# Optimization experiments

Measured on AMD Instinct MI355X. Metric: run time of the kernel, lower is better.

The kernel has to match this reference:

```python
import jax, jax.numpy as jnp
import numpy as np

B, T, C = 32, 128, 64
E, H = 8, 4            # feat_dim, num_heads
D = E // H             # head_dim = 2
HID = 32               # hidden_dim


def setup_inputs() -> dict:
    key = jax.random.key(0)
    ks = jax.random.split(key, 20)
    s = 0.1
    return {
        "x": jax.random.normal(ks[0], (B, T, C), jnp.float32),
        # input_proj: Linear(C, C)
        "W_in": jax.random.normal(ks[1], (C, C), jnp.float32) * s,
        "b_in": jax.random.normal(ks[2], (C,), jnp.float32) * s,
        # time_step_score: Linear(C, C//4) -> GELU -> Linear(C//4, 1) -> Sigmoid
        "W_ts1": jax.random.normal(ks[3], (C // 4, C), jnp.float32) * s,
        "b_ts1": jax.random.normal(ks[4], (C // 4,), jnp.float32) * s,
        "W_ts2": jax.random.normal(ks[5], (1, C // 4), jnp.float32) * s,
        "b_ts2": jax.random.normal(ks[6], (1,), jnp.float32) * s,
        # per-channel GRU(1 -> E): torch gate order (r, z, n)
        "W_ih": jax.random.normal(ks[7], (C, 3 * E), jnp.float32) * s,      # input size 1
        "W_hh": jax.random.normal(ks[8], (C, 3 * E, E), jnp.float32) * s,
        "b_ih": jax.random.normal(ks[9], (C, 3 * E), jnp.float32) * s,
        "b_hh": jax.random.normal(ks[10], (C, 3 * E), jnp.float32) * s,
        # shared MultiheadAttention(E, 4): packed in_proj + out_proj
        "W_qkv": jax.random.normal(ks[11], (3 * E, E), jnp.float32) * s,
        "b_qkv": jax.random.normal(ks[12], (3 * E,), jnp.float32) * s,
        "W_o": jax.random.normal(ks[13], (E, E), jnp.float32) * s,
        "b_o": jax.random.normal(ks[14], (E,), jnp.float32) * s,
        # out_proj: Linear(C*E, HID)
        "W_out": jax.random.normal(ks[15], (HID, C * E), jnp.float32) * s,
        "b_out": jax.random.normal(ks[16], (HID,), jnp.float32) * s,
    }


def _forward(x, W_in, b_in, W_ts1, b_ts1, W_ts2, b_ts2,
             W_ih, W_hh, b_ih, b_hh, W_qkv, b_qkv, W_o, b_o, W_out, b_out):
    bs, ts, c = x.shape
    # time step importance: per-timestep MLP over the raw features
    h1 = jax.nn.gelu(jnp.einsum('btc,fc->btf', x, W_ts1) + b_ts1, approximate=False)
    ts_imp = jax.nn.sigmoid(jnp.einsum('btf,of->bto', h1, W_ts2) + b_ts2)[..., 0]  # [B,T]

    xp = jnp.einsum('btc,dc->btd', x, W_in) + b_in  # [B,T,C]

    # Batched per-channel GRU scan over time. state h: [B,C,E]
    def step(h, x_t):
        gi = x_t[:, :, None] * W_ih[None] + b_ih          # [B,C,3E]
        gh = jnp.einsum('bce,cge->bcg', h, W_hh) + b_hh   # [B,C,3E]
        ir, iz, inn = gi[..., :E], gi[..., E:2 * E], gi[..., 2 * E:]
        hr, hz, hn = gh[..., :E], gh[..., E:2 * E], gh[..., 2 * E:]
        r = jax.nn.sigmoid(ir + hr)
        z = jax.nn.sigmoid(iz + hz)
        n = jnp.tanh(inn + r * hn)
        h_new = (1.0 - z) * n + z * h
        return h_new, h_new

    h0 = jnp.zeros((bs, c, E), xp.dtype)
    _, hs = jax.lax.scan(step, h0, jnp.transpose(xp, (1, 0, 2)))  # [T,B,C,E]
    hs_bcte = jnp.transpose(hs, (1, 2, 0, 3))                     # [B,C,T,E]

    # Shared MHA applied independently per channel (batched over B*C)
    qkv = jnp.einsum('bcte,fe->bctf', hs_bcte, W_qkv) + b_qkv     # [B,C,T,3E]
    q, k, v = qkv[..., :E], qkv[..., E:2 * E], qkv[..., 2 * E:]
    def heads(t):
        return t.reshape(bs, c, ts, H, D)
    q, k, v = heads(q), heads(k), heads(v)
    scores = jnp.einsum('bcthd,bcshd->bchts', q, k) / np.sqrt(D)
    attn = jax.nn.softmax(scores, axis=-1)
    o = jnp.einsum('bchts,bcshd->bcthd', attn, v).reshape(bs, c, ts, E)
    attn_out = jnp.einsum('bcte,fe->bctf', o, W_o) + b_o          # [B,C,T,E]
    attention = jnp.transpose(attn_out, (0, 2, 1, 3))             # [B,T,C,E]

    out_flat = jnp.transpose(hs, (1, 0, 2, 3)).reshape(bs, ts, c * E)  # [B,T,C*E]
    out = jnp.einsum('btf,hf->bth', out_flat, W_out) + b_out           # [B,T,HID]

    feat_imp = jax.nn.sigmoid(attention.sum(axis=(1, 3)))   # [B,C]
    tsf_imp = jax.nn.sigmoid(attention.sum(axis=-1))        # [B,T,C]
    return out[:, -1, :], feat_imp, ts_imp, tsf_imp


def reference(x, W_in, b_in, W_ts1, b_ts1, W_ts2, b_ts2,
              W_ih, W_hh, b_ih, b_hh, W_qkv, b_qkv, W_o, b_o, W_out, b_out):
    return _forward(x, W_in, b_in, W_ts1, b_ts1, W_ts2, b_ts2,
                    W_ih, W_hh, b_ih, b_hh, W_qkv, b_qkv, W_o, b_o, W_out, b_out)
```

## Files before the change

### kernel.cpp

```cpp
#include <hip/hip_runtime.h>
#include <hip/hip_bf16.h>
#include <math.h>

#define B_ 32
#define T_ 128
#define C_ 64
#define E_ 8
#define HID_ 32

__device__ __forceinline__ float sigmoidf_(float x) { return 1.0f / (1.0f + __expf(-x)); }
__device__ __forceinline__ float tanhf_(float x) {
    float xc = fminf(fmaxf(x, -15.0f), 15.0f);
    float e = __expf(2.0f * xc);
    return (e - 1.0f) / (e + 1.0f);
}

__global__ __launch_bounds__(64) void k_gru(
    const float* __restrict__ x, const float* __restrict__ W_in, const float* __restrict__ b_in,
    const float* __restrict__ W_ih, const float* __restrict__ W_hh,
    const float* __restrict__ b_ih, const float* __restrict__ b_hh,
    float* __restrict__ hs, float* __restrict__ fh)
{
    const int tid = threadIdx.x;
    const int ci = tid >> 3;
    const int e = tid & 7;
    const int chain = blockIdx.x * 8 + ci;
    const int b = chain >> 6;
    const int c = chain & 63;

    __shared__ float wsh[8][C_];
    __shared__ float xc[8][T_ + 1];

#pragma unroll
    for (int i = 0; i < 8; ++i) {
        int idx = tid * 8 + i;
        int ci2 = idx >> 6;
        int cc = (blockIdx.x * 8 + ci2) & 63;
        wsh[ci2][idx & 63] = W_in[cc * C_ + (idx & 63)];
    }
    __syncthreads();

    const float bi = b_in[c];
    for (int tt = 0; tt < 16; ++tt) {
        const int t = e * 16 + tt;
        const float4* xr = (const float4*)(x + (b * T_ + t) * C_);
        float a = bi;
#pragma unroll
        for (int k4 = 0; k4 < 16; ++k4) {
            float4 xv = xr[k4];
            a = fmaf(xv.x, wsh[ci][k4 * 4 + 0], a);
            a = fmaf(xv.y, wsh[ci][k4 * 4 + 1], a);
            a = fmaf(xv.z, wsh[ci][k4 * 4 + 2], a);
            a = fmaf(xv.w, wsh[ci][k4 * 4 + 3], a);
        }
        xc[ci][t] = a;
    }
    __syncthreads();

    float wr[E_], wz[E_], wn[E_];
#pragma unroll
    for (int j = 0; j < E_; ++j) {
        wr[j] = W_hh[(c * 24 + 0 * E_ + e) * E_ + j];
        wz[j] = W_hh[(c * 24 + 1 * E_ + e) * E_ + j];
        wn[j] = W_hh[(c * 24 + 2 * E_ + e) * E_ + j];
    }
    const float wir = W_ih[c * 24 + e], wiz = W_ih[c * 24 + E_ + e], win = W_ih[c * 24 + 2 * E_ + e];
    const float bir = b_ih[c * 24 + e], biz = b_ih[c * 24 + E_ + e], bin_ = b_ih[c * 24 + 2 * E_ + e];
    const float bhr = b_hh[c * 24 + e], bhz = b_hh[c * 24 + E_ + e], bhn = b_hh[c * 24 + 2 * E_ + e];

    float h = 0.0f;
    float* ho = hs + (size_t)chain * T_ * E_ + e;
    for (int t = 0; t < T_; ++t) {
        float xv = xc[ci][t];
        float gr = fmaf(xv, wir, bir) + bhr;
        float gz = fmaf(xv, wiz, biz) + bhz;
        float gn = fmaf(xv, win, bin_);
        float hn = bhn;
#pragma unroll
        for (int j = 0; j < E_; ++j) {
            float hj = __shfl(h, j, E_);
            gr = fmaf(hj, wr[j], gr);
            gz = fmaf(hj, wz[j], gz);
            hn = fmaf(hj, wn[j], hn);
        }
        float r = sigmoidf_(gr);
        float z = sigmoidf_(gz);
        float nn = tanhf_(fmaf(r, hn, gn));
        h = (1.0f - z) * nn + z * h;
        ho[t * E_] = h;
    }
    fh[chain * E_ + e] = h;
}

__global__ __launch_bounds__(256) void k_attn(
    const float* __restrict__ hs, const float* __restrict__ W_qkv, const float* __restrict__ b_qkv,
    const float* __restrict__ W_o, const float* __restrict__ b_o,
    float* __restrict__ feat_imp, float* __restrict__ tsf_imp)
{
    const int bc = blockIdx.x;
    const int b = bc >> 6, c = bc & 63;
    const int tid = threadIdx.x;
    const int t = tid & 127;
    const int p = tid >> 7;

    __shared__ __align__(16) float ks[T_][E_];
    __shared__ __align__(16) float vs[T_][E_];
    __shared__ __align__(16) float pacc[T_][12];
    __shared__ float wssum[E_];
    __shared__ float bsum_s;
    __shared__ float red[T_];

    float hrow[E_];
    {
        const float4* hp = (const float4*)(hs + (size_t)bc * T_ * E_ + t * E_);
        float4 h0 = hp[0], h1 = hp[1];
        hrow[0] = h0.x; hrow[1] = h0.y; hrow[2] = h0.z; hrow[3] = h0.w;
        hrow[4] = h1.x; hrow[5] = h1.y; hrow[6] = h1.z; hrow[7] = h1.w;
    }

    const float qscale = 0.70710678118654752f * 1.44269504088896341f;
    float q[E_];
#pragma unroll
    for (int f = 0; f < E_; ++f) {
        float a = b_qkv[f];
#pragma unroll
        for (int j = 0; j < E_; ++j) a = fmaf(hrow[j], W_qkv[f * E_ + j], a);
        q[f] = a * qscale;
    }
    if (p == 0) {
#pragma unroll
        for (int f = 0; f < E_; ++f) {
            float a = b_qkv[E_ + f];
#pragma unroll
            for (int j = 0; j < E_; ++j) a = fmaf(hrow[j], W_qkv[(E_ + f) * E_ + j], a);
            ks[t][f] = a;
        }
    } else {
#pragma unroll
        for (int f = 0; f < E_; ++f) {
            float a = b_qkv[2 * E_ + f];
#pragma unroll
            for (int j = 0; j < E_; ++j) a = fmaf(hrow[j], W_qkv[(2 * E_ + f) * E_ + j], a);
            vs[t][f] = a;
        }
    }
    if (tid < E_) {
        float ws = 0.0f;
#pragma unroll
        for (int fp = 0; fp < E_; ++fp) ws += W_o[fp * E_ + tid];
        wssum[tid] = ws;
    }
    if (tid == E_) {
        float bs = 0.0f;
#pragma unroll
        for (int fp = 0; fp < E_; ++fp) bs += b_o[fp];
        bsum_s = bs;
    }
    __syncthreads();

    float l[4] = {0.f, 0.f, 0.f, 0.f};
    float acc[E_] = {0.f, 0.f, 0.f, 0.f, 0.f, 0.f, 0.f, 0.f};
    const int s0 = p * 64;
    for (int s = s0; s < s0 + 64; ++s) {
        float4 k0 = *(const float4*)&ks[s][0];
        float4 k1 = *(const float4*)&ks[s][4];
        float4 v0 = *(const float4*)&vs[s][0];
        float4 v1 = *(const float4*)&vs[s][4];
        float p0 = exp2f(fmaf(q[1], k0.y, q[0] * k0.x));
        float p1 = exp2f(fmaf(q[3], k0.w, q[2] * k0.z));
        float p2 = exp2f(fmaf(q[5], k1.y, q[4] * k1.x));
        float p3 = exp2f(fmaf(q[7], k1.w, q[6] * k1.z));
        l[0] += p0; l[1] += p1; l[2] += p2; l[3] += p3;
        acc[0] = fmaf(p0, v0.x, acc[0]); acc[1] = fmaf(p0, v0.y, acc[1]);
        acc[2] = fmaf(p1, v0.z, acc[2]); acc[3] = fmaf(p1, v0.w, acc[3]);
        acc[4] = fmaf(p2, v1.x, acc[4]); acc[5] = fmaf(p2, v1.y, acc[5]);
        acc[6] = fmaf(p3, v1.z, acc[6]); acc[7] = fmaf(p3, v1.w, acc[7]);
    }

    if (p == 1) {
#pragma unroll
        for (int i = 0; i < 4; ++i) pacc[t][i] = l[i];
#pragma unroll
        for (int j = 0; j < 8; ++j) pacc[t][4 + j] = acc[j];
    }
    __syncthreads();

    if (p == 0) {
#pragma unroll
        for (int i = 0; i < 4; ++i) l[i] += pacc[t][i];
#pragma unroll
        for (int j = 0; j < 8; ++j) acc[j] += pacc[t][4 + j];
        float S = bsum_s;
#pragma unroll
        for (int f = 0; f < E_; ++f) S = fmaf(acc[f] / l[f >> 1], wssum[f], S);
        tsf_imp[(size_t)b * T_ * C_ + (size_t)t * C_ + c] = sigmoidf_(S);
        red[t] = S;
    }
    __syncthreads();
    for (int off = 64; off > 0; off >>= 1) {
        if (p == 0 && t < off) red[t] += red[t + off];
        __syncthreads();
    }
    if (tid == 0) feat_imp[bc] = sigmoidf_(red[0]);
}

__global__ __launch_bounds__(64) void k_ts(
    const float* __restrict__ x,
    const float* __restrict__ W_ts1, const float* __restrict__ b_ts1,
    const float* __restrict__ W_ts2, const float* __restrict__ b_ts2,
    float* __restrict__ ts_imp)
{
    const int bt = blockIdx.x;
    const int tid = threadIdx.x;
    __shared__ float xs[C_];
    __shared__ float h1[16];
    xs[tid] = x[bt * C_ + tid];
    __syncthreads();
    if (tid < 16) {
        float a = b_ts1[tid];
#pragma unroll
        for (int k = 0; k < C_; ++k) a = fmaf(xs[k], W_ts1[tid * C_ + k], a);
        h1[tid] = 0.5f * a * (1.0f + erff(a * 0.70710678118654752f));
    }
    __syncthreads();
    if (tid == 0) {
        float s = b_ts2[0];
#pragma unroll
        for (int k = 0; k < 16; ++k) s = fmaf(h1[k], W_ts2[k], s);
        ts_imp[bt] = sigmoidf_(s);
    }
}

__global__ __launch_bounds__(64) void k_out(
    const float* __restrict__ fh, const float* __restrict__ W_out, const float* __restrict__ b_out,
    float* __restrict__ out0)
{
    const int b = blockIdx.x;
    const int tid = threadIdx.x;
    __shared__ float hf[C_ * E_];
    const float4* src = (const float4*)(fh + (b * C_ + tid) * E_);
    float4* dst = (float4*)(hf + tid * E_);
    dst[0] = src[0];
    dst[1] = src[1];
    __syncthreads();
    if (tid < HID_) {
        float a = b_out[tid];
        const float* wo = W_out + tid * (C_ * E_);
        for (int k = 0; k < C_ * E_; ++k) a = fmaf(hf[k], wo[k], a);
        out0[b * HID_ + tid] = a;
    }
}

extern "C" void kernel_launch(void* const* d_in, const int* in_sizes, int n_in,
                              void* d_out, int out_size, void* d_ws, size_t ws_size,
                              hipStream_t stream) {
    (void)in_sizes; (void)n_in; (void)out_size; (void)ws_size;

    float* out0 = (float*)d_out;
    float* feat = out0 + B_ * HID_;
    float* tsim = feat + B_ * C_;
    float* tsf  = tsim + B_ * T_;

    const float* x     = (const float*)d_in[0];
    const float* W_in  = (const float*)d_in[1];
    const float* b_in  = (const float*)d_in[2];
    const float* W_ts1 = (const float*)d_in[3];
    const float* b_ts1 = (const float*)d_in[4];
    const float* W_ts2 = (const float*)d_in[5];
    const float* b_ts2 = (const float*)d_in[6];
    const float* W_ih  = (const float*)d_in[7];
    const float* W_hh  = (const float*)d_in[8];
    const float* b_ih  = (const float*)d_in[9];
    const float* b_hh  = (const float*)d_in[10];
    const float* W_qkv = (const float*)d_in[11];
    const float* b_qkv = (const float*)d_in[12];
    const float* W_o   = (const float*)d_in[13];
    const float* b_o   = (const float*)d_in[14];
    const float* W_out = (const float*)d_in[15];
    const float* b_out = (const float*)d_in[16];

    float* fhb = (float*)d_ws;
    float* hsb = fhb + B_ * C_ * E_;

    hipLaunchKernelGGL(k_gru, dim3(B_ * C_ / 8), dim3(64), 0, stream,
                       x, W_in, b_in, W_ih, W_hh, b_ih, b_hh, hsb, fhb);
    hipLaunchKernelGGL(k_attn, dim3(B_ * C_), dim3(256), 0, stream,
                       hsb, W_qkv, b_qkv, W_o, b_o, feat, tsf);
    hipLaunchKernelGGL(k_ts, dim3(B_ * T_), dim3(64), 0, stream,
                       x, W_ts1, b_ts1, W_ts2, b_ts2, tsim);
    hipLaunchKernelGGL(k_out, dim3(B_), dim3(64), 0, stream,
                       fhb, W_out, b_out, out0);
}
```

Measured before the change: 101.8 us.

## Halve attention block threads with two queries per thread and fast math intrinsics

The attention kernel now runs 128 threads per (b,c) instead of 256. Each thread computes K/V for one row, then handles two query rows over half the key range. The two halves are combined with xor shuffles instead of a shared-memory partial buffer and an extra barrier, so each K/V shared load is reused across two queries. Sigmoid and tanh in the GRU and elsewhere now use exp2 plus a hardware reciprocal, and the GRU update is folded into one fma; this trims the serial recurrence latency but slightly reduces numerical accuracy.

```diff
diff --git a/kernel.cpp b/kernel.cpp
--- a/kernel.cpp
+++ b/kernel.cpp
@@ -8,11 +8,16 @@
 #define E_ 8
 #define HID_ 32
 
-__device__ __forceinline__ float sigmoidf_(float x) { return 1.0f / (1.0f + __expf(-x)); }
-__device__ __forceinline__ float tanhf_(float x) {
+#define LOG2E 1.44269504088896341f
+
+__device__ __forceinline__ float fast_rcp(float x) { return __builtin_amdgcn_rcpf(x); }
+__device__ __forceinline__ float fast_sigmoid(float x) {
+    return fast_rcp(1.0f + exp2f(-LOG2E * x));
+}
+__device__ __forceinline__ float fast_tanh(float x) {
     float xc = fminf(fmaxf(x, -15.0f), 15.0f);
-    float e = __expf(2.0f * xc);
-    return (e - 1.0f) / (e + 1.0f);
+    float t = exp2f(2.0f * LOG2E * xc);
+    return (t - 1.0f) * fast_rcp(t + 1.0f);
 }
 
 __global__ __launch_bounds__(64) void k_gru(
@@ -83,16 +88,16 @@
             gz = fmaf(hj, wz[j], gz);
             hn = fmaf(hj, wn[j], hn);
         }
-        float r = sigmoidf_(gr);
-        float z = sigmoidf_(gz);
-        float nn = tanhf_(fmaf(r, hn, gn));
-        h = (1.0f - z) * nn + z * h;
+        float r = fast_sigmoid(gr);
+        float z = fast_sigmoid(gz);
+        float nn = fast_tanh(fmaf(r, hn, gn));
+        h = fmaf(z, h - nn, nn);
         ho[t * E_] = h;
     }
     fh[chain * E_ + e] = h;
 }
 
-__global__ __launch_bounds__(256) void k_attn(
+__global__ __launch_bounds__(128) void k_attn(
     const float* __restrict__ hs, const float* __restrict__ W_qkv, const float* __restrict__ b_qkv,
     const float* __restrict__ W_o, const float* __restrict__ b_o,
     float* __restrict__ feat_imp, float* __restrict__ tsf_imp)
@@ -100,108 +105,128 @@
     const int bc = blockIdx.x;
     const int b = bc >> 6, c = bc & 63;
     const int tid = threadIdx.x;
-    const int t = tid & 127;
-    const int p = tid >> 7;
-
+    const int r = tid >> 1;
+    const int p = tid & 1;
+
+    __shared__ __align__(16) float hsl[T_][E_];
     __shared__ __align__(16) float ks[T_][E_];
     __shared__ __align__(16) float vs[T_][E_];
-    __shared__ __align__(16) float pacc[T_][12];
     __shared__ float wssum[E_];
     __shared__ float bsum_s;
     __shared__ float red[T_];
 
-    float hrow[E_];
     {
-        const float4* hp = (const float4*)(hs + (size_t)bc * T_ * E_ + t * E_);
-        float4 h0 = hp[0], h1 = hp[1];
-        hrow[0] = h0.x; hrow[1] = h0.y; hrow[2] = h0.z; hrow[3] = h0.w;
-        hrow[4] = h1.x; hrow[5] = h1.y; hrow[6] = h1.z; hrow[7] = h1.w;
-    }
-
-    const float qscale = 0.70710678118654752f * 1.44269504088896341f;
-    float q[E_];
-#pragma unroll
-    for (int f = 0; f < E_; ++f) {
-        float a = b_qkv[f];
-#pragma unroll
-        for (int j = 0; j < E_; ++j) a = fmaf(hrow[j], W_qkv[f * E_ + j], a);
-        q[f] = a * qscale;
-    }
-    if (p == 0) {
+        const float4* hp = (const float4*)(hs + (size_t)bc * T_ * E_ + tid * E_);
+        ((float4*)&hsl[tid][0])[0] = hp[0];
+        ((float4*)&hsl[tid][0])[1] = hp[1];
+    }
+    if (tid < E_) {
+        float ws = 0.0f;
+#pragma unroll
+        for (int fp = 0; fp < E_; ++fp) ws += W_o[fp * E_ + tid];
+        wssum[tid] = ws;
+    }
+    if (tid == E_) {
+        float bs = 0.0f;
+#pragma unroll
+        for (int fp = 0; fp < E_; ++fp) bs += b_o[fp];
+        bsum_s = bs;
+    }
+    __syncthreads();
+
+    const float qscale = 0.70710678118654752f * LOG2E;
+    {
+        float hr[E_];
+#pragma unroll
+        for (int j = 0; j < E_; ++j) hr[j] = hsl[tid][j];
 #pragma unroll
         for (int f = 0; f < E_; ++f) {
             float a = b_qkv[E_ + f];
 #pragma unroll
-            for (int j = 0; j < E_; ++j) a = fmaf(hrow[j], W_qkv[(E_ + f) * E_ + j], a);
-            ks[t][f] = a;
-        }
-    } else {
+            for (int j = 0; j < E_; ++j) a = fmaf(hr[j], W_qkv[(E_ + f) * E_ + j], a);
+            ks[tid][f] = a;
+        }
 #pragma unroll
         for (int f = 0; f < E_; ++f) {
             float a = b_qkv[2 * E_ + f];
 #pragma unroll
-            for (int j = 0; j < E_; ++j) a = fmaf(hrow[j], W_qkv[(2 * E_ + f) * E_ + j], a);
-            vs[t][f] = a;
-        }
-    }
-    if (tid < E_) {
-        float ws = 0.0f;
-#pragma unroll
-        for (int fp = 0; fp < E_; ++fp) ws += W_o[fp * E_ + tid];
-        wssum[tid] = ws;
-    }
-    if (tid == E_) {
-        float bs = 0.0f;
-#pragma unroll
-        for (int fp = 0; fp < E_; ++fp) bs += b_o[fp];
-        bsum_s = bs;
-    }
-    __syncthreads();
-
-    float l[4] = {0.f, 0.f, 0.f, 0.f};
-    float acc[E_] = {0.f, 0.f, 0.f, 0.f, 0.f, 0.f, 0.f, 0.f};
-    const int s0 = p * 64;
-    for (int s = s0; s < s0 + 64; ++s) {
-        float4 k0 = *(const float4*)&ks[s][0];
-        float4 k1 = *(const float4*)&ks[s][4];
-        float4 v0 = *(const float4*)&vs[s][0];
-        float4 v1 = *(const float4*)&vs[s][4];
-        float p0 = exp2f(fmaf(q[1], k0.y, q[0] * k0.x));
-        float p1 = exp2f(fmaf(q[3], k0.w, q[2] * k0.z));
-        float p2 = exp2f(fmaf(q[5], k1.y, q[4] * k1.x));
-        float p3 = exp2f(fmaf(q[7], k1.w, q[6] * k1.z));
-        l[0] += p0; l[1] += p1; l[2] += p2; l[3] += p3;
-        acc[0] = fmaf(p0, v0.x, acc[0]); acc[1] = fmaf(p0, v0.y, acc[1]);
-        acc[2] = fmaf(p1, v0.z, acc[2]); acc[3] = fmaf(p1, v0.w, acc[3]);
-        acc[4] = fmaf(p2, v1.x, acc[4]); acc[5] = fmaf(p2, v1.y, acc[5]);
-        acc[6] = fmaf(p3, v1.z, acc[6]); acc[7] = fmaf(p3, v1.w, acc[7]);
-    }
-
-    if (p == 1) {
-#pragma unroll
-        for (int i = 0; i < 4; ++i) pacc[t][i] = l[i];
-#pragma unroll
-        for (int j = 0; j < 8; ++j) pacc[t][4 + j] = acc[j];
-    }
-    __syncthreads();
-
-    if (p == 0) {
-#pragma unroll
-        for (int i = 0; i < 4; ++i) l[i] += pacc[t][i];
-#pragma unroll
-        for (int j = 0; j < 8; ++j) acc[j] += pacc[t][4 + j];
-        float S = bsum_s;
-#pragma unroll
-        for (int f = 0; f < E_; ++f) S = fmaf(acc[f] / l[f >> 1], wssum[f], S);
-        tsf_imp[(size_t)b * T_ * C_ + (size_t)t * C_ + c] = sigmoidf_(S);
-        red[t] = S;
-    }
+            for (int j = 0; j < E_; ++j) a = fmaf(hr[j], W_qkv[(2 * E_ + f) * E_ + j], a);
+            vs[tid][f] = a;
+        }
+    }
+    float q0[E_], q1[E_];
+#pragma unroll
+    for (int f = 0; f < E_; ++f) {
+        float a0 = b_qkv[f], a1 = b_qkv[f];
+#pragma unroll
+        for (int j = 0; j < E_; ++j) {
+            float w = W_qkv[f * E_ + j];
+            a0 = fmaf(hsl[r][j], w, a0);
+            a1 = fmaf(hsl[r + 64][j], w, a1);
+        }
+        q0[f] = a0 * qscale;
+        q1[f] = a1 * qscale;
+    }
+    __syncthreads();
+
+    float l0[4] = {0.f,0.f,0.f,0.f}, l1[4] = {0.f,0.f,0.f,0.f};
+    float a0[E_] = {0.f,0.f,0.f,0.f,0.f,0.f,0.f,0.f};
+    float a1[E_] = {0.f,0.f,0.f,0.f,0.f,0.f,0.f,0.f};
+    const float* kb = &ks[p * 64][0];
+    const float* vb = &vs[p * 64][0];
+#pragma unroll 8
+    for (int i = 0; i < 64; ++i) {
+        float4 k0 = *(const float4*)(kb + i * 8);
+        float4 k1 = *(const float4*)(kb + i * 8 + 4);
+        float4 v0 = *(const float4*)(vb + i * 8);
+        float4 v1 = *(const float4*)(vb + i * 8 + 4);
+        float p00 = exp2f(fmaf(q0[1], k0.y, q0[0] * k0.x));
+        float p01 = exp2f(fmaf(q0[3], k0.w, q0[2] * k0.z));
+        float p02 = exp2f(fmaf(q0[5], k1.y, q0[4] * k1.x));
+        float p03 = exp2f(fmaf(q0[7], k1.w, q0[6] * k1.z));
+        float p10 = exp2f(fmaf(q1[1], k0.y, q1[0] * k0.x));
+        float p11 = exp2f(fmaf(q1[3], k0.w, q1[2] * k0.z));
+        float p12 = exp2f(fmaf(q1[5], k1.y, q1[4] * k1.x));
+        float p13 = exp2f(fmaf(q1[7], k1.w, q1[6] * k1.z));
+        l0[0] += p00; l0[1] += p01; l0[2] += p02; l0[3] += p03;
+        l1[0] += p10; l1[1] += p11; l1[2] += p12; l1[3] += p13;
+        a0[0] = fmaf(p00, v0.x, a0[0]); a0[1] = fmaf(p00, v0.y, a0[1]);
+        a0[2] = fmaf(p01, v0.z, a0[2]); a0[3] = fmaf(p01, v0.w, a0[3]);
+        a0[4] = fmaf(p02, v1.x, a0[4]); a0[5] = fmaf(p02, v1.y, a0[5]);
+        a0[6] = fmaf(p03, v1.z, a0[6]); a0[7] = fmaf(p03, v1.w, a0[7]);
+        a1[0] = fmaf(p10, v0.x, a1[0]); a1[1] = fmaf(p10, v0.y, a1[1]);
+        a1[2] = fmaf(p11, v0.z, a1[2]); a1[3] = fmaf(p11, v0.w, a1[3]);
+        a1[4] = fmaf(p12, v1.x, a1[4]); a1[5] = fmaf(p12, v1.y, a1[5]);
+        a1[6] = fmaf(p13, v1.z, a1[6]); a1[7] = fmaf(p13, v1.w, a1[7]);
+    }
+
+#pragma unroll
+    for (int i = 0; i < 4; ++i) {
+        l0[i] += __shfl_xor(l0[i], 1);
+        l1[i] += __shfl_xor(l1[i], 1);
+    }
+#pragma unroll
+    for (int j = 0; j < E_; ++j) {
+        a0[j] += __shfl_xor(a0[j], 1);
+        a1[j] += __shfl_xor(a1[j], 1);
+    }
+
+    const float* lm = p ? l1 : l0;
+    const float* am = p ? a1 : a0;
+    const int row = p ? (r + 64) : r;
+    float S = bsum_s;
+#pragma unroll
+    for (int f = 0; f < E_; ++f)
+        S = fmaf(am[f] * fast_rcp(lm[f >> 1]), wssum[f], S);
+
+    tsf_imp[(size_t)b * T_ * C_ + (size_t)row * C_ + c] = fast_sigmoid(S);
+    red[row] = S;
     __syncthreads();
     for (int off = 64; off > 0; off >>= 1) {
-        if (p == 0 && t < off) red[t] += red[t + off];
+        if (tid < off) red[tid] += red[tid + off];
         __syncthreads();
     }
-    if (tid == 0) feat_imp[bc] = sigmoidf_(red[0]);
+    if (tid == 0) feat_imp[bc] = fast_sigmoid(red[0]);
 }
 
 __global__ __launch_bounds__(64) void k_ts(
@@ -227,7 +252,7 @@
         float s = b_ts2[0];
 #pragma unroll
         for (int k = 0; k < 16; ++k) s = fmaf(h1[k], W_ts2[k], s);
-        ts_imp[bt] = sigmoidf_(s);
+        ts_imp[bt] = fast_sigmoid(s);
     }
 }
 
@@ -284,7 +309,7 @@
 
     hipLaunchKernelGGL(k_gru, dim3(B_ * C_ / 8), dim3(64), 0, stream,
                        x, W_in, b_in, W_ih, W_hh, b_ih, b_hh, hsb, fhb);
-    hipLaunchKernelGGL(k_attn, dim3(B_ * C_), dim3(256), 0, stream,
+    hipLaunchKernelGGL(k_attn, dim3(B_ * C_), dim3(128), 0, stream,
                        hsb, W_qkv, b_qkv, W_o, b_o, feat, tsf);
     hipLaunchKernelGGL(k_ts, dim3(B_ * T_), dim3(64), 0, stream,
                        x, W_ts1, b_ts1, W_ts2, b_ts2, tsim);
```

After: 110.6 us. +8.7%, slower.

## Fold W_o column sums into V and use fast reciprocal sigmoid/tanh

Applied to the files above, without the earlier changes.

In the attention kernel, each head's V pair is pre-combined with the summed W_o columns into one scalar per head. The softmax-weighted accumulation then needs 4 accumulators instead of 8, V shared memory shrinks, and the partial-sum exchange is smaller. The W_o sums are computed before the QKV projection so they are ready when V is folded. Separately, the sigmoid and tanh helpers switch to exp2 plus a hardware reciprocal, and the GRU state update becomes a single fma, trading a little precision for fewer instructions.

```diff
diff --git a/kernel.cpp b/kernel.cpp
--- a/kernel.cpp
+++ b/kernel.cpp
@@ -8,11 +8,16 @@
 #define E_ 8
 #define HID_ 32
 
-__device__ __forceinline__ float sigmoidf_(float x) { return 1.0f / (1.0f + __expf(-x)); }
-__device__ __forceinline__ float tanhf_(float x) {
+#define LOG2E 1.44269504088896341f
+
+__device__ __forceinline__ float fast_rcp(float x) { return __builtin_amdgcn_rcpf(x); }
+__device__ __forceinline__ float fast_sigmoid(float x) {
+    return fast_rcp(1.0f + exp2f(-LOG2E * x));
+}
+__device__ __forceinline__ float fast_tanh(float x) {
     float xc = fminf(fmaxf(x, -15.0f), 15.0f);
-    float e = __expf(2.0f * xc);
-    return (e - 1.0f) / (e + 1.0f);
+    float t = exp2f(2.0f * LOG2E * xc);
+    return (t - 1.0f) * fast_rcp(t + 1.0f);
 }
 
 __global__ __launch_bounds__(64) void k_gru(
@@ -83,10 +88,10 @@
             gz = fmaf(hj, wz[j], gz);
             hn = fmaf(hj, wn[j], hn);
         }
-        float r = sigmoidf_(gr);
-        float z = sigmoidf_(gz);
-        float nn = tanhf_(fmaf(r, hn, gn));
-        h = (1.0f - z) * nn + z * h;
+        float r = fast_sigmoid(gr);
+        float z = fast_sigmoid(gz);
+        float nn = fast_tanh(fmaf(r, hn, gn));
+        h = fmaf(z, h - nn, nn);
         ho[t * E_] = h;
     }
     fh[chain * E_ + e] = h;
@@ -104,11 +109,25 @@
     const int p = tid >> 7;
 
     __shared__ __align__(16) float ks[T_][E_];
-    __shared__ __align__(16) float vs[T_][E_];
-    __shared__ __align__(16) float pacc[T_][12];
+    __shared__ __align__(16) float us[T_][4];
+    __shared__ __align__(16) float pacc[T_][8];
     __shared__ float wssum[E_];
     __shared__ float bsum_s;
     __shared__ float red[T_];
+
+    if (tid < E_) {
+        float ws = 0.0f;
+#pragma unroll
+        for (int fp = 0; fp < E_; ++fp) ws += W_o[fp * E_ + tid];
+        wssum[tid] = ws;
+    }
+    if (tid == E_) {
+        float bs = 0.0f;
+#pragma unroll
+        for (int fp = 0; fp < E_; ++fp) bs += b_o[fp];
+        bsum_s = bs;
+    }
+    __syncthreads();
 
     float hrow[E_];
     {
@@ -118,7 +137,7 @@
         hrow[4] = h1.x; hrow[5] = h1.y; hrow[6] = h1.z; hrow[7] = h1.w;
     }
 
-    const float qscale = 0.70710678118654752f * 1.44269504088896341f;
+    const float qscale = 0.70710678118654752f * LOG2E;
     float q[E_];
 #pragma unroll
     for (int f = 0; f < E_; ++f) {
@@ -136,64 +155,53 @@
             ks[t][f] = a;
         }
     } else {
+        float v[E_];
 #pragma unroll
         for (int f = 0; f < E_; ++f) {
             float a = b_qkv[2 * E_ + f];
 #pragma unroll
             for (int j = 0; j < E_; ++j) a = fmaf(hrow[j], W_qkv[(2 * E_ + f) * E_ + j], a);
-            vs[t][f] = a;
+            v[f] = a;
         }
-    }
-    if (tid < E_) {
-        float ws = 0.0f;
-#pragma unroll
-        for (int fp = 0; fp < E_; ++fp) ws += W_o[fp * E_ + tid];
-        wssum[tid] = ws;
-    }
-    if (tid == E_) {
-        float bs = 0.0f;
-#pragma unroll
-        for (int fp = 0; fp < E_; ++fp) bs += b_o[fp];
-        bsum_s = bs;
+#pragma unroll
+        for (int hh = 0; hh < 4; ++hh)
+            us[t][hh] = fmaf(v[2 * hh + 1], wssum[2 * hh + 1], v[2 * hh] * wssum[2 * hh]);
     }
     __syncthreads();
 
     float l[4] = {0.f, 0.f, 0.f, 0.f};
-    float acc[E_] = {0.f, 0.f, 0.f, 0.f, 0.f, 0.f, 0.f, 0.f};
-    const int s0 = p * 64;
-    for (int s = s0; s < s0 + 64; ++s) {
-        float4 k0 = *(const float4*)&ks[s][0];
-        float4 k1 = *(const float4*)&ks[s][4];
-        float4 v0 = *(const float4*)&vs[s][0];
-        float4 v1 = *(const float4*)&vs[s][4];
+    float S4[4] = {0.f, 0.f, 0.f, 0.f};
+    const float* kb = &ks[p * 64][0];
+    const float* ub = &us[p * 64][0];
+#pragma unroll 16
+    for (int i = 0; i < 64; ++i) {
+        float4 k0 = *(const float4*)(kb + i * 8);
+        float4 k1 = *(const float4*)(kb + i * 8 + 4);
+        float4 uu = *(const float4*)(ub + i * 4);
         float p0 = exp2f(fmaf(q[1], k0.y, q[0] * k0.x));
         float p1 = exp2f(fmaf(q[3], k0.w, q[2] * k0.z));
         float p2 = exp2f(fmaf(q[5], k1.y, q[4] * k1.x));
         float p3 = exp2f(fmaf(q[7], k1.w, q[6] * k1.z));
         l[0] += p0; l[1] += p1; l[2] += p2; l[3] += p3;
-        acc[0] = fmaf(p0, v0.x, acc[0]); acc[1] = fmaf(p0, v0.y, acc[1]);
-        acc[2] = fmaf(p1, v0.z, acc[2]); acc[3] = fmaf(p1, v0.w, acc[3]);
-        acc[4] = fmaf(p2, v1.x, acc[4]); acc[5] = fmaf(p2, v1.y, acc[5]);
-        acc[6] = fmaf(p3, v1.z, acc[6]); acc[7] = fmaf(p3, v1.w, acc[7]);
+        S4[0] = fmaf(p0, uu.x, S4[0]);
+        S4[1] = fmaf(p1, uu.y, S4[1]);
+        S4[2] = fmaf(p2, uu.z, S4[2]);
+        S4[3] = fmaf(p3, uu.w, S4[3]);
     }
 
     if (p == 1) {
 #pragma unroll
-        for (int i = 0; i < 4; ++i) pacc[t][i] = l[i];
-#pragma unroll
-        for (int j = 0; j < 8; ++j) pacc[t][4 + j] = acc[j];
+        for (int i = 0; i < 4; ++i) { pacc[t][i] = l[i]; pacc[t][4 + i] = S4[i]; }
     }
     __syncthreads();
 
     if (p == 0) {
 #pragma unroll
-        for (int i = 0; i < 4; ++i) l[i] += pacc[t][i];
-#pragma unroll
-        for (int j = 0; j < 8; ++j) acc[j] += pacc[t][4 + j];
+        for (int i = 0; i < 4; ++i) { l[i] += pacc[t][i]; S4[i] += pacc[t][4 + i]; }
         float S = bsum_s;
 #pragma unroll
-        for (int f = 0; f < E_; ++f) S = fmaf(acc[f] / l[f >> 1], wssum[f], S);
-        tsf_imp[(size_t)b * T_ * C_ + (size_t)t * C_ + c] = sigmoidf_(S);
+        for (int hh = 0; hh < 4; ++hh) S = fmaf(S4[hh], fast_rcp(l[hh]), S);
+        tsf_imp[(size_t)b * T_ * C_ + (size_t)t * C_ + c] = fast_sigmoid(S);
         red[t] = S;
     }
     __syncthreads();
@@ -201,7 +209,7 @@
         if (p == 0 && t < off) red[t] += red[t + off];
         __syncthreads();
     }
-    if (tid == 0) feat_imp[bc] = sigmoidf_(red[0]);
+    if (tid == 0) feat_imp[bc] = fast_sigmoid(red[0]);
 }
 
 __global__ __launch_bounds__(64) void k_ts(
@@ -227,7 +235,7 @@
         float s = b_ts2[0];
 #pragma unroll
         for (int k = 0; k < 16; ++k) s = fmaf(h1[k], W_ts2[k], s);
-        ts_imp[bt] = sigmoidf_(s);
+        ts_imp[bt] = fast_sigmoid(s);
     }
 }
 
```

Result: faster. 94.27 us (-7.4%).
